# Kernel optimization log

Hardware: AMD Instinct MI355X
Metric: run time of the kernel (lower is better)

The kernel has to match this reference:

```python
import jax, jax.numpy as jnp
import numpy as np

D = 1024           # input_size
D2 = 2 * D         # hidden width of the three inner linears
OUT = 1024         # output_size
S = 8192           # tokens per example


def setup_inputs() -> dict:
    key = jax.random.key(0)
    ks = jax.random.split(key, 11)
    def lin(k, fan_in, fan_out):
        bound = 1.0 / np.sqrt(fan_in)
        kw, kb = jax.random.split(k)
        W = jax.random.uniform(kw, (fan_in, fan_out), jnp.float32, -bound, bound)
        b = jax.random.uniform(kb, (fan_out,), jnp.float32, -bound, bound)
        return W, b
    W_in, b_in = lin(ks[0], D, D2)      # reading_example_input
    W_out, b_out = lin(ks[1], D, D2)    # reading_example_output
    W_cat, b_cat = lin(ks[2], D2, D2)   # concatenated_layer_map
    W_fin, b_fin = lin(ks[3], D2, OUT)  # final_map
    return {
        "input_embedding": jax.random.normal(ks[4], (1, S, D), jnp.float32),
        "output_embedding": jax.random.normal(ks[5], (1, S, D), jnp.float32),
        "random_augmentation": jax.random.normal(ks[6], (1, S, D), jnp.float32),
        "W_in": W_in, "b_in": b_in,
        "W_out": W_out, "b_out": b_out,
        "W_cat": W_cat, "b_cat": b_cat,
        "W_fin": W_fin, "b_fin": b_fin,
    }


def reference(input_embedding, output_embedding, random_augmentation,
              W_in, b_in, W_out, b_out, W_cat, b_cat, W_fin, b_fin):
    def march(x, y):
        # x, y: [1, S, D]
        iq = jax.nn.softmax(x @ W_in + b_in, axis=-1)[0]    # [S, 2D]
        oq = jax.nn.softmax(y @ W_out + b_out, axis=-1)[0]  # [S, 2D]
        cat = jnp.concatenate((x, y), axis=-1)[0]           # [S, 2D]
        icm = jax.nn.softmax(cat @ W_cat + b_cat, axis=-1)  # [S, 2D]
        iqk = iq.T @ icm                                    # [2D, 2D]
        oqk = oq.T @ icm                                    # [2D, 2D]
        meta = jax.nn.relu(iqk @ oqk.T)                     # [2D, 2D]
        scale = jnp.sqrt(jnp.float32(icm.shape[-1]))
        res = (icm @ meta) / scale                          # [S, 2D]
        return jax.nn.relu(res @ W_fin + b_fin)             # [S, OUT]

    transformation = march(input_embedding, output_embedding)
    random_desc = march(input_embedding, random_augmentation)
    return (transformation, random_desc)
```

## Files before the change

### kernel.cpp

```cpp
#include <hip/hip_runtime.h>

#define S_TOK 8192
#define DIM   1024
#define DIM2  2048
#define OUTN  1024

typedef __bf16 bf16x8 __attribute__((ext_vector_type(8)));
typedef float  f32x4  __attribute__((ext_vector_type(4)));
typedef short  s16x8  __attribute__((ext_vector_type(8)));
typedef unsigned short u16x4 __attribute__((ext_vector_type(4)));

__device__ __forceinline__ unsigned short f2bf(float x) {
  unsigned u = __builtin_bit_cast(unsigned, x);
  u = (u + 0x7FFFu + ((u >> 16) & 1u)) >> 16;
  return (unsigned short)u;
}
__device__ __forceinline__ float bf2f(unsigned short u) {
  return __builtin_bit_cast(float, (unsigned)u << 16);
}

__device__ __forceinline__ void gld_lds16(const void* g, void* l) {
  auto* g1 = reinterpret_cast<__attribute__((address_space(1))) unsigned*>(
      (unsigned long long)g);
  auto* l3 = reinterpret_cast<__attribute__((address_space(3))) unsigned*>(
      (unsigned long long)l);
  __builtin_amdgcn_global_load_lds(g1, l3, 16, 0, 0);
}

__device__ __forceinline__ int lds_off(int idx, int k) {
  int b = (idx << 7) + (k << 1);
  b ^= ((idx ^ (idx >> 3)) & 7) << 4;
  return b;
}

struct CvtTab { const float* in[3]; unsigned short* out[3]; };
__global__ __launch_bounds__(256) void cvt_f32_bf16_3(CvtTab t) {
  const float* in = t.in[blockIdx.y];
  unsigned short* out = t.out[blockIdx.y];
  int i = blockIdx.x * 256 + threadIdx.x;
  float4 v = ((const float4*)in)[i];
  u16x4 o;
  o[0] = f2bf(v.x); o[1] = f2bf(v.y); o[2] = f2bf(v.z); o[3] = f2bf(v.w);
  *(u16x4*)(out + (size_t)i * 4) = o;
}

struct WtTab { const float* in[4]; unsigned short* out[4]; int R[4]; int C[4]; };
__global__ __launch_bounds__(256) void transpose_w4(WtTab t) {
  const int z = blockIdx.z;
  const int R = t.R[z], C = t.C[z];
  const int r0 = blockIdx.y << 6, c0 = blockIdx.x << 6;
  if (r0 >= R || c0 >= C) return;
  const float* in = t.in[z];
  unsigned short* out = t.out[z];
  __shared__ unsigned short tl[64 * 64];
  const int tid = threadIdx.x;
#pragma unroll
  for (int i = 0; i < 2; ++i) {
    int ch = tid + (i << 8);
    int r = ch >> 3, c8 = (ch & 7) << 3;
    const float* p = in + (size_t)(r0 + r) * C + c0 + c8;
    float4 a = *(const float4*)p, b = *(const float4*)(p + 4);
    s16x8 w;
    w[0] = (short)f2bf(a.x); w[1] = (short)f2bf(a.y);
    w[2] = (short)f2bf(a.z); w[3] = (short)f2bf(a.w);
    w[4] = (short)f2bf(b.x); w[5] = (short)f2bf(b.y);
    w[6] = (short)f2bf(b.z); w[7] = (short)f2bf(b.w);
    int sw = ((r ^ (r >> 3)) & 7) << 3;
    *(s16x8*)&tl[(r << 6) + (c8 ^ sw)] = w;
  }
  __syncthreads();
#pragma unroll
  for (int i = 0; i < 2; ++i) {
    int ch = tid + (i << 8);
    int c = ch >> 3, r8 = (ch & 7) << 3;
    s16x8 w;
#pragma unroll
    for (int j = 0; j < 8; ++j) {
      int rr = r8 + j;
      w[j] = (short)tl[(rr << 6) + (c ^ (((rr ^ (rr >> 3)) & 7) << 3))];
    }
    *(s16x8*)(out + (size_t)(c0 + c) * R + r0 + r8) = w;
  }
}

struct SmTab { unsigned short* T[6]; };
__global__ __launch_bounds__(512) void softmax_cols(SmTab tab) {
  unsigned short* T = tab.T[blockIdx.y];
  const int tid = threadIdx.x;
  const int colg = tid & 63, seg = tid >> 6;
  const size_t c = ((size_t)blockIdx.x << 6) + colg;
  float m = -1e30f, s = 0.f;
  for (int n = seg; n < DIM2; n += 8) {
    float v = bf2f(T[(size_t)n * S_TOK + c]);
    float mn = fmaxf(m, v);
    s = s * __expf(m - mn) + __expf(v - mn);
    m = mn;
  }
  __shared__ float redm[512], reds[512];
  redm[tid] = m; reds[tid] = s;
  __syncthreads();
  if (seg == 0) {
    float M = m, S = s;
#pragma unroll
    for (int k = 1; k < 8; ++k) {
      float mk = redm[colg + (k << 6)], sk = reds[colg + (k << 6)];
      float mn = fmaxf(M, mk);
      S = S * __expf(M - mn) + sk * __expf(mk - mn);
      M = mn;
    }
    redm[colg] = M; reds[colg] = 1.0f / S;
  }
  __syncthreads();
  m = redm[colg];
  const float inv = reds[colg];
  for (int n = seg; n < DIM2; n += 8) {
    size_t idx = (size_t)n * S_TOK + c;
    T[idx] = f2bf(__expf(bf2f(T[idx]) - m) * inv);
  }
}

struct GPtr {
  const unsigned short* A[6];
  const unsigned short* Arow2[6];
  const unsigned short* B[6];
  const unsigned short* Bk2[6];
  const float* bias[6];
  void* C[6];
  int Ks[6];
  int ldas[6];
};
struct TPar { const unsigned short* src[2]; unsigned short* dst[2]; };

template <int BIAS_ROW, int OUT_BF16, int NZG>
__global__ __launch_bounds__(256, 3) void gemm_nt(GPtr p, TPar tp, int ldb, int ldc,
                                                  float scale, int do_relu) {
  __shared__ __align__(16) char lds[32768];
  const int z = blockIdx.z;
  const int tid  = threadIdx.x;

  if (NZG >= 0 && z >= NZG) {
    const unsigned short* src = tp.src[z - NZG];
    unsigned short* dst = tp.dst[z - NZG];
    unsigned short* tl = (unsigned short*)lds;
    const int nblk = gridDim.x * gridDim.y;
    int bid = blockIdx.y * gridDim.x + blockIdx.x;
    for (int it = bid; it < (DIM2 / 64) * (S_TOK / 64); it += nblk) {
      int tx = it & (S_TOK / 64 - 1), ty = it >> 7;
      int r0 = ty << 6, c0 = tx << 6;
#pragma unroll
      for (int i = 0; i < 2; ++i) {
        int ch = tid + (i << 8);
        int r = ch >> 3, c8 = (ch & 7) << 3;
        s16x8 w = *(const s16x8*)(src + (size_t)(r0 + r) * S_TOK + c0 + c8);
        int sw = ((r ^ (r >> 3)) & 7) << 3;
        *(s16x8*)&tl[(r << 6) + (c8 ^ sw)] = w;
      }
      __syncthreads();
#pragma unroll
      for (int i = 0; i < 2; ++i) {
        int ch = tid + (i << 8);
        int c = ch >> 3, r8 = (ch & 7) << 3;
        s16x8 w;
#pragma unroll
        for (int j = 0; j < 8; ++j) {
          int rr = r8 + j;
          w[j] = (short)tl[(rr << 6) + (c ^ (((rr ^ (rr >> 3)) & 7) << 3))];
        }
        *(s16x8*)(dst + (size_t)(c0 + c) * DIM2 + r0 + r8) = w;
      }
      __syncthreads();
    }
    return;
  }

  char* As = lds;
  char* Bs = lds + 16384;
  const int lane = tid & 63;
  const int wave = tid >> 6;
  const int wm = (wave >> 1) << 6;
  const int wn = (wave & 1) << 6;
  const int m0 = blockIdx.y << 7;
  const int n0 = blockIdx.x << 7;
  const int lda = p.ldas[z];
  const int K = p.Ks[z];

  const unsigned short* Au = p.A[z];
  const unsigned short* B  = p.B[z];
  const float* bias = p.bias[z];
  void* Cv = p.C[z];

  int srow[4], sgk[4];
#pragma unroll
  for (int i = 0; i < 4; ++i) {
    int c = (wave << 8) + (i << 6) + lane;
    int row = c >> 3, kc = c & 7;
    srow[i] = row;
    sgk[i]  = (kc ^ ((row ^ (row >> 3)) & 7)) << 3;
  }

  f32x4 acc[4][4];
#pragma unroll
  for (int i = 0; i < 4; ++i)
#pragma unroll
    for (int j = 0; j < 4; ++j) acc[i][j] = {0.f, 0.f, 0.f, 0.f};

  for (int k0 = 0; k0 < K; k0 += 64) {
#pragma unroll
    for (int i = 0; i < 4; ++i) {
      char* dA = As + (((wave << 2) + i) << 10);
      char* dB = Bs + (((wave << 2) + i) << 10);
      gld_lds16(Au + (size_t)(m0 + srow[i]) * lda + k0 + sgk[i], dA);
      gld_lds16(B  + (size_t)(n0 + srow[i]) * ldb + k0 + sgk[i], dB);
    }
    __syncthreads();
#pragma unroll
    for (int ks = 0; ks < 2; ++ks) {
      bf16x8 af[4], bfr[4];
      int kk = (ks << 5) + ((lane >> 4) << 3);
#pragma unroll
      for (int t = 0; t < 4; ++t) {
        af[t]  = *(const bf16x8*)(As + lds_off(wm + (t << 4) + (lane & 15), kk));
        bfr[t] = *(const bf16x8*)(Bs + lds_off(wn + (t << 4) + (lane & 15), kk));
      }
#pragma unroll
      for (int mt = 0; mt < 4; ++mt)
#pragma unroll
        for (int nt = 0; nt < 4; ++nt)
          acc[mt][nt] = __builtin_amdgcn_mfma_f32_16x16x32_bf16(af[mt], bfr[nt], acc[mt][nt], 0, 0, 0);
    }
    __syncthreads();
  }

  if (OUT_BF16) {
    unsigned short* ct = (unsigned short*)lds;
    __syncthreads();
#pragma unroll
    for (int nt = 0; nt < 4; ++nt) {
      int cl = wn + (nt << 4) + (lane & 15);
      float bcol = (!BIAS_ROW && bias) ? bias[n0 + cl] : 0.0f;
#pragma unroll
      for (int mt = 0; mt < 4; ++mt) {
#pragma unroll
        for (int r = 0; r < 4; ++r) {
          int rl = wm + (mt << 4) + ((lane >> 4) << 2) + r;
          float bv = BIAS_ROW ? (bias ? bias[m0 + rl] : 0.0f) : bcol;
          float v = acc[mt][nt][r] * scale + bv;
          if (do_relu) v = fmaxf(v, 0.0f);
          ct[(rl << 7) + (cl ^ (((rl >> 2) & 3) << 4))] = f2bf(v);
        }
      }
    }
    __syncthreads();
#pragma unroll
    for (int it = 0; it < 8; ++it) {
      int c = (it << 8) + tid;
      int rl = c >> 4, co = (c & 15) << 3;
      s16x8 w = *(const s16x8*)(ct + (rl << 7) + (co ^ (((rl >> 2) & 3) << 4)));
      *(s16x8*)((unsigned short*)Cv + (size_t)(m0 + rl) * ldc + n0 + co) = w;
    }
  } else {
#pragma unroll
    for (int nt = 0; nt < 4; ++nt) {
      int col = n0 + wn + (nt << 4) + (lane & 15);
      float bcol = (!BIAS_ROW && bias) ? bias[col] : 0.0f;
#pragma unroll
      for (int mt = 0; mt < 4; ++mt) {
        f32x4 a = acc[mt][nt];
#pragma unroll
        for (int r = 0; r < 4; ++r) {
          int rowg = m0 + wm + (mt << 4) + ((lane >> 4) << 2) + r;
          float bv = BIAS_ROW ? (bias ? bias[rowg] : 0.0f) : bcol;
          float v = a[r] * scale + bv;
          if (do_relu) v = fmaxf(v, 0.0f);
          ((float*)Cv)[(size_t)rowg * ldc + col] = v;
        }
      }
    }
  }
}

template <int ASPLIT, int BSPLIT, int BIAS_ROW, int OUT_BF16>
__global__ __launch_bounds__(512, 2) void gemm256(GPtr p, int ldb, int ldc,
                                                  float scale, int do_relu,
                                                  int RW, int XW) {
  __shared__ __align__(16) char lds[131072];
  const int z = blockIdx.z;
  const int tid  = threadIdx.x;
  const int lane = tid & 63;
  const int wave = tid >> 6;
  const int wm   = wave >> 2;
  const int wn   = wave & 3;
  const int lda  = p.ldas[z];
  const int K    = p.Ks[z];

  const int gx = gridDim.x;
  const int nper = (gx * gridDim.y) >> 3;
  const int RH = nper / RW;
  int bid = blockIdx.y * gx + blockIdx.x;
  int xcd = bid & 7, j = bid >> 3;
  const int n0 = (RW * (xcd % XW) + (j % RW)) << 8;
  const int m0 = (RH * (xcd / XW) + (j / RW)) << 8;

  const unsigned short* Au = p.A[z];
  int mb = m0;
  if (ASPLIT && m0 >= 2048) { Au = p.Arow2[z]; mb = m0 - 2048; }
  const unsigned short* Bp = p.B[z];
  const float* bias = p.bias[z];
  void* Cv = p.C[z];

  const int NT = K >> 6;

  int srow_[2], skel_[2];
#pragma unroll
  for (int i = 0; i < 2; ++i) {
    int row = (i << 7) + (wave << 4) + (lane >> 2);
    srow_[i] = row;
    skel_[i] = ((lane & 3) ^ ((row >> 1) & 3)) << 3;
  }
  const unsigned short* aB[2];
  const unsigned short* bB[2];
  const unsigned short* b2B[2];
#pragma unroll
  for (int i = 0; i < 2; ++i) {
    aB[i]  = Au + (size_t)(mb + srow_[i]) * lda + skel_[i];
    bB[i]  = Bp + (size_t)(n0 + srow_[i]) * ldb + skel_[i];
    b2B[i] = BSPLIT ? (p.Bk2[z] + (size_t)(n0 + srow_[i]) * ldb + skel_[i] - DIM)
                    : bB[i];
  }

  auto stage_unit = [&](int t, int u) {
    const int k0 = t << 6;
    const int h  = u >> 1;
    char* base = lds + ((t & 1) << 16) + ((u & 1) << 15) + (h << 14) + (wave << 10);
#pragma unroll
    for (int i = 0; i < 2; ++i) {
      const unsigned short* src;
      if (u & 1) src = ((BSPLIT && k0 >= DIM) ? b2B[i] : bB[i]) + k0 + (h << 5);
      else       src = aB[i] + k0 + (h << 5);
      gld_lds16(src, base + (i << 13));
    }
  };

  auto rdA = [&](const char* buf, int h, int mf) -> bf16x8 {
    int row = (wm << 7) + (mf << 4) + (lane & 15);
    int col = (lane >> 4) ^ ((row >> 1) & 3);
    return *(const bf16x8*)(buf + (h << 14) + (row << 6) + (col << 4));
  };
  auto rdB = [&](const char* buf, int h, int nf) -> bf16x8 {
    int row = (wn << 6) + (nf << 4) + (lane & 15);
    int col = (lane >> 4) ^ ((row >> 1) & 3);
    return *(const bf16x8*)(buf + 32768 + (h << 14) + (row << 6) + (col << 4));
  };

  f32x4 acc[8][4];
#pragma unroll
  for (int i = 0; i < 8; ++i)
#pragma unroll
    for (int j2 = 0; j2 < 4; ++j2) acc[i][j2] = {0.f, 0.f, 0.f, 0.f};

  stage_unit(0, 0); stage_unit(0, 1); stage_unit(0, 2); stage_unit(0, 3);

  for (int t = 0; t < NT; ++t) {
    const char* buf = lds + ((t & 1) << 16);
    const bool more = (t + 1 < NT);
    bf16x8 aq[4], bq[4];

    if (more) { stage_unit(t + 1, 0); asm volatile("s_waitcnt vmcnt(6)" ::: "memory"); }
    else      { asm volatile("s_waitcnt vmcnt(4)" ::: "memory"); }
    __builtin_amdgcn_s_barrier();
    __builtin_amdgcn_sched_barrier(0);
#pragma unroll
    for (int nf = 0; nf < 4; ++nf) bq[nf] = rdB(buf, 0, nf);
#pragma unroll
    for (int mf = 0; mf < 4; ++mf) aq[mf] = rdA(buf, 0, mf);
    __builtin_amdgcn_s_setprio(1);
#pragma unroll
    for (int mf = 0; mf < 4; ++mf)
#pragma unroll
      for (int nf = 0; nf < 4; ++nf)
        acc[mf][nf] = __builtin_amdgcn_mfma_f32_16x16x32_bf16(aq[mf], bq[nf], acc[mf][nf], 0, 0, 0);
    __builtin_amdgcn_s_setprio(0);
    __builtin_amdgcn_s_barrier();

#pragma unroll
    for (int mf = 0; mf < 4; ++mf) aq[mf] = rdA(buf, 0, mf + 4);
    if (more) stage_unit(t + 1, 1);
    __builtin_amdgcn_s_setprio(1);
#pragma unroll
    for (int mf = 0; mf < 4; ++mf)
#pragma unroll
      for (int nf = 0; nf < 4; ++nf)
        acc[mf + 4][nf] = __builtin_amdgcn_mfma_f32_16x16x32_bf16(aq[mf], bq[nf], acc[mf + 4][nf], 0, 0, 0);
    __builtin_amdgcn_s_setprio(0);
    __builtin_amdgcn_s_barrier();

    if (more) { stage_unit(t + 1, 2); asm volatile("s_waitcnt vmcnt(6)" ::: "memory"); }
    else      { asm volatile("s_waitcnt vmcnt(0)" ::: "memory"); }
    __builtin_amdgcn_s_barrier();
    __builtin_amdgcn_sched_barrier(0);
#pragma unroll
    for (int nf = 0; nf < 4; ++nf) bq[nf] = rdB(buf, 1, nf);
#pragma unroll
    for (int mf = 0; mf < 4; ++mf) aq[mf] = rdA(buf, 1, mf);
    __builtin_amdgcn_s_setprio(1);
#pragma unroll
    for (int mf = 0; mf < 4; ++mf)
#pragma unroll
      for (int nf = 0; nf < 4; ++nf)
        acc[mf][nf] = __builtin_amdgcn_mfma_f32_16x16x32_bf16(aq[mf], bq[nf], acc[mf][nf], 0, 0, 0);
    __builtin_amdgcn_s_setprio(0);
    __builtin_amdgcn_s_barrier();

#pragma unroll
    for (int mf = 0; mf < 4; ++mf) aq[mf] = rdA(buf, 1, mf + 4);
    if (more) stage_unit(t + 1, 3);
    __builtin_amdgcn_s_setprio(1);
#pragma unroll
    for (int mf = 0; mf < 4; ++mf)
#pragma unroll
      for (int nf = 0; nf < 4; ++nf)
        acc[mf + 4][nf] = __builtin_amdgcn_mfma_f32_16x16x32_bf16(aq[mf], bq[nf], acc[mf + 4][nf], 0, 0, 0);
    __builtin_amdgcn_s_setprio(0);
    __builtin_amdgcn_s_barrier();
  }

  __syncthreads();
  if (OUT_BF16) {
    unsigned short* ct = (unsigned short*)lds;
#pragma unroll
    for (int nf = 0; nf < 4; ++nf) {
      int cl = (wn << 6) + (nf << 4) + (lane & 15);
      float bcol = (!BIAS_ROW && bias) ? bias[n0 + cl] : 0.0f;
#pragma unroll
      for (int mf = 0; mf < 8; ++mf) {
#pragma unroll
        for (int r = 0; r < 4; ++r) {
          int rl = (wm << 7) + (mf << 4) + ((lane >> 4) << 2) + r;
          float bv = BIAS_ROW ? (bias ? bias[m0 + rl] : 0.0f) : bcol;
          float v = acc[mf][nf][r] * scale + bv;
          if (do_relu) v = fmaxf(v, 0.0f);
          ct[(rl << 8) + (cl ^ (((rl >> 2) & 3) << 4))] = f2bf(v);
        }
      }
    }
    __syncthreads();
#pragma unroll
    for (int it = 0; it < 16; ++it) {
      int c = (it << 9) + tid;
      int rl = c >> 5, co = (c & 31) << 3;
      s16x8 w = *(const s16x8*)(ct + (rl << 8) + (co ^ (((rl >> 2) & 3) << 4)));
      *(s16x8*)((unsigned short*)Cv + (size_t)(m0 + rl) * ldc + n0 + co) = w;
    }
  } else {
    float* ctf = (float*)lds;
#pragma unroll
    for (int h = 0; h < 2; ++h) {
      if (h) __syncthreads();
      if (wm == h) {
#pragma unroll
        for (int nf = 0; nf < 4; ++nf) {
          int cl = (wn << 6) + (nf << 4) + (lane & 15);
          float bcol = (!BIAS_ROW && bias) ? bias[n0 + cl] : 0.0f;
#pragma unroll
          for (int mf = 0; mf < 8; ++mf) {
#pragma unroll
            for (int r = 0; r < 4; ++r) {
              int rl2 = (mf << 4) + ((lane >> 4) << 2) + r;
              float bv = BIAS_ROW ? (bias ? bias[m0 + (h << 7) + rl2] : 0.0f) : bcol;
              float v = acc[mf][nf][r] * scale + bv;
              if (do_relu) v = fmaxf(v, 0.0f);
              ctf[(rl2 << 8) + (cl ^ (((rl2 >> 2) & 3) << 3))] = v;
            }
          }
        }
      }
      __syncthreads();
#pragma unroll
      for (int it = 0; it < 16; ++it) {
        int c = (it << 9) + tid;
        int rl2 = c >> 6, co = (c & 63) << 2;
        float4 w = *(const float4*)(ctf + (rl2 << 8) + (co ^ (((rl2 >> 2) & 3) << 3)));
        *(float4*)((float*)Cv + (size_t)(m0 + (h << 7) + rl2) * ldc + n0 + co) = w;
      }
    }
  }
}

extern "C" void kernel_launch(void* const* d_in, const int* in_sizes, int n_in,
                              void* d_out, int out_size, void* d_ws, size_t ws_size,
                              hipStream_t stream) {
  const float* X   = (const float*)d_in[0];
  const float* Y   = (const float*)d_in[1];
  const float* R   = (const float*)d_in[2];
  const float* Wi  = (const float*)d_in[3];
  const float* bi  = (const float*)d_in[4];
  const float* Wo  = (const float*)d_in[5];
  const float* bo  = (const float*)d_in[6];
  const float* Wc  = (const float*)d_in[7];
  const float* bc  = (const float*)d_in[8];
  const float* Wf  = (const float*)d_in[9];
  const float* bf_ = (const float*)d_in[10];
  float* out = (float*)d_out;

  char* ws = (char*)d_ws;
  size_t off = 0;
  auto alloc = [&](size_t b) { char* p = ws + off; off += (b + 255) & ~(size_t)255; return p; };
  unsigned short* Xb   = (unsigned short*)alloc((size_t)S_TOK * DIM  * 2);
  unsigned short* Yb   = (unsigned short*)alloc((size_t)S_TOK * DIM  * 2);
  unsigned short* Rb   = (unsigned short*)alloc((size_t)S_TOK * DIM  * 2);
  unsigned short* WiT  = (unsigned short*)alloc((size_t)DIM2 * DIM  * 2);
  unsigned short* WoT  = (unsigned short*)alloc((size_t)DIM2 * DIM  * 2);
  unsigned short* WcT  = (unsigned short*)alloc((size_t)DIM2 * DIM2 * 2);
  unsigned short* WfT  = (unsigned short*)alloc((size_t)OUTN * DIM2 * 2);
  unsigned short* iqT  = (unsigned short*)alloc((size_t)DIM2 * S_TOK * 2);
  unsigned short* oqT0 = (unsigned short*)alloc((size_t)DIM2 * S_TOK * 2);
  unsigned short* oqT1 = (unsigned short*)alloc((size_t)DIM2 * S_TOK * 2);
  unsigned short* icmT0= (unsigned short*)alloc((size_t)DIM2 * S_TOK * 2);
  unsigned short* icmT1= (unsigned short*)alloc((size_t)DIM2 * S_TOK * 2);
  unsigned short* iqk0 = Xb;
  unsigned short* oqk0 = Xb + (size_t)DIM2*DIM2;
  unsigned short* iqk1 = Yb;
  unsigned short* oqk1 = Yb + (size_t)DIM2*DIM2;
  unsigned short* meta0= iqT;
  unsigned short* meta1= iqT + (size_t)DIM2*DIM2;
  unsigned short* MWT0 = iqT + (size_t)2*DIM2*DIM2;
  unsigned short* MWT1 = iqT + (size_t)2*DIM2*DIM2 + (size_t)OUTN*DIM2;
  unsigned short* icm0 = oqT0;
  unsigned short* icm1 = oqT1;

  {
    CvtTab t{};
    t.in[0] = X; t.in[1] = Y; t.in[2] = R;
    t.out[0] = Xb; t.out[1] = Yb; t.out[2] = Rb;
    cvt_f32_bf16_3<<<dim3((S_TOK * DIM / 4) / 256, 3), 256, 0, stream>>>(t);
  }
  {
    WtTab t{};
    t.in[0] = Wi; t.out[0] = WiT; t.R[0] = DIM;  t.C[0] = DIM2;
    t.in[1] = Wo; t.out[1] = WoT; t.R[1] = DIM;  t.C[1] = DIM2;
    t.in[2] = Wc; t.out[2] = WcT; t.R[2] = DIM2; t.C[2] = DIM2;
    t.in[3] = Wf; t.out[3] = WfT; t.R[3] = DIM2; t.C[3] = OUTN;
    transpose_w4<<<dim3(32, 32, 4), 256, 0, stream>>>(t);
  }

  const float rscale = 0.022097086912079608f;

  {
    GPtr g{};
    g.A[0] = WcT; g.B[0] = Xb; g.Bk2[0] = Yb; g.bias[0] = bc; g.C[0] = icmT0;
    g.Ks[0] = DIM2; g.ldas[0] = DIM2;
    g.A[1] = WcT; g.B[1] = Xb; g.Bk2[1] = Rb; g.bias[1] = bc; g.C[1] = icmT1;
    g.Ks[1] = DIM2; g.ldas[1] = DIM2;
    g.A[2] = WiT; g.B[2] = Xb; g.Bk2[2] = Xb; g.bias[2] = bi; g.C[2] = iqT;
    g.Ks[2] = DIM; g.ldas[2] = DIM;
    g.A[3] = WoT; g.B[3] = Yb; g.Bk2[3] = Yb; g.bias[3] = bo; g.C[3] = oqT0;
    g.Ks[3] = DIM; g.ldas[3] = DIM;
    g.A[4] = WoT; g.B[4] = Rb; g.Bk2[4] = Rb; g.bias[4] = bo; g.C[4] = oqT1;
    g.Ks[4] = DIM; g.ldas[4] = DIM;
    gemm256<0,1,1,1><<<dim3(S_TOK/256, DIM2/256, 5), 512, 0, stream>>>(
        g, DIM, S_TOK, 1.f, 0, 4, 8);
  }
  {
    SmTab st{};
    st.T[0] = iqT; st.T[1] = oqT0; st.T[2] = oqT1; st.T[3] = icmT0; st.T[4] = icmT1;
    softmax_cols<<<dim3(S_TOK / 64, 5), dim3(512), 0, stream>>>(st);
  }
  {
    GPtr g{};
    g.A[0] = iqT; g.A[1] = iqT;
    g.Arow2[0] = oqT0; g.Arow2[1] = oqT1;
    g.B[0] = icmT0; g.B[1] = icmT1;
    g.C[0] = iqk0; g.C[1] = iqk1;
    g.Ks[0] = S_TOK; g.Ks[1] = S_TOK;
    g.ldas[0] = S_TOK; g.ldas[1] = S_TOK;
    gemm256<1,0,0,1><<<dim3(DIM2/256, 4096/256, 2), 512, 0, stream>>>(
        g, S_TOK, DIM2, 1.f, 0, 4, 2);
  }
  {
    GPtr g{};
    g.A[0] = iqk0; g.B[0] = oqk0; g.C[0] = meta0; g.Ks[0] = DIM2; g.ldas[0] = DIM2;
    g.A[1] = iqk1; g.B[1] = oqk1; g.C[1] = meta1; g.Ks[1] = DIM2; g.ldas[1] = DIM2;
    TPar tp{};
    tp.src[0] = icmT0; tp.dst[0] = icm0;
    tp.src[1] = icmT1; tp.dst[1] = icm1;
    gemm_nt<0,1,2><<<dim3(DIM2/128, DIM2/128, 4), 256, 0, stream>>>(
        g, tp, DIM2, DIM2, 1.f, 1);
  }
  {
    GPtr g{};
    g.A[0] = WfT; g.B[0] = meta0; g.C[0] = MWT0; g.Ks[0] = DIM2; g.ldas[0] = DIM2;
    g.A[1] = WfT; g.B[1] = meta1; g.C[1] = MWT1; g.Ks[1] = DIM2; g.ldas[1] = DIM2;
    TPar tp{};
    gemm_nt<0,1,2><<<dim3(DIM2/128, OUTN/128, 2), 256, 0, stream>>>(
        g, tp, DIM2, DIM2, rscale, 0);
  }
  {
    GPtr g{};
    g.A[0] = icm0; g.B[0] = MWT0; g.bias[0] = bf_; g.C[0] = out;
    g.Ks[0] = DIM2; g.ldas[0] = DIM2;
    g.A[1] = icm1; g.B[1] = MWT1; g.bias[1] = bf_;
    g.C[1] = out + (size_t)S_TOK * OUTN;
    g.Ks[1] = DIM2; g.ldas[1] = DIM2;
    gemm256<0,0,0,0><<<dim3(OUTN/256, S_TOK/256, 2), 512, 0, stream>>>(
        g, DIM2, OUTN, 1.f, 1, 4, 1);
  }
  (void)in_sizes; (void)n_in; (void)out_size; (void)ws_size;
}
```

Before: 893.0 us.

## Merge prep kernels, cache softmax column values, add two-phase GEMM pipeline variant

Fuses the activation bf16 conversion and the weight transpose into one launch to save a kernel launch. The column softmax now keeps its loaded values in registers (32 x 8 bf16 per thread), so the normalisation pass does not re-read global memory. A PHASES template parameter adds a two-phase main-loop schedule to the first projection GEMM, with fewer barriers and larger register fragments; the other GEMMs keep the four-phase schedule. The risks are higher register pressure in softmax and in the two-phase GEMM, and a mostly idle grid in the merged prep kernel.

```diff
diff --git a/kernel.cpp b/kernel.cpp
--- a/kernel.cpp
+++ b/kernel.cpp
@@ -33,27 +33,31 @@
   return b;
 }
 
-struct CvtTab { const float* in[3]; unsigned short* out[3]; };
-__global__ __launch_bounds__(256) void cvt_f32_bf16_3(CvtTab t) {
-  const float* in = t.in[blockIdx.y];
-  unsigned short* out = t.out[blockIdx.y];
-  int i = blockIdx.x * 256 + threadIdx.x;
-  float4 v = ((const float4*)in)[i];
-  u16x4 o;
-  o[0] = f2bf(v.x); o[1] = f2bf(v.y); o[2] = f2bf(v.z); o[3] = f2bf(v.w);
-  *(u16x4*)(out + (size_t)i * 4) = o;
-}
-
-struct WtTab { const float* in[4]; unsigned short* out[4]; int R[4]; int C[4]; };
-__global__ __launch_bounds__(256) void transpose_w4(WtTab t) {
-  const int z = blockIdx.z;
-  const int R = t.R[z], C = t.C[z];
-  const int r0 = blockIdx.y << 6, c0 = blockIdx.x << 6;
-  if (r0 >= R || c0 >= C) return;
-  const float* in = t.in[z];
-  unsigned short* out = t.out[z];
+struct PrepTab {
+  const float* in[3]; unsigned short* out[3];
+  const float* win[4]; unsigned short* wout[4]; int R[4]; int C[4];
+};
+__global__ __launch_bounds__(256) void prep_all(PrepTab t) {
   __shared__ unsigned short tl[64 * 64];
   const int tid = threadIdx.x;
+  if (blockIdx.z < 3) {
+    const float* in = t.in[blockIdx.z];
+    unsigned short* out = t.out[blockIdx.z];
+    int i = blockIdx.x * 256 + tid;
+    float4 v = ((const float4*)in)[i];
+    u16x4 o;
+    o[0] = f2bf(v.x); o[1] = f2bf(v.y); o[2] = f2bf(v.z); o[3] = f2bf(v.w);
+    *(u16x4*)(out + (size_t)i * 4) = o;
+    return;
+  }
+  int x = blockIdx.x;
+  if (x >= 4096) return;
+  int wz = x >> 10, rem = x & 1023, bx = rem & 31, by = rem >> 5;
+  const int R = t.R[wz], C = t.C[wz];
+  const int r0 = by << 6, c0 = bx << 6;
+  if (r0 >= R || c0 >= C) return;
+  const float* in = t.win[wz];
+  unsigned short* out = t.wout[wz];
 #pragma unroll
   for (int i = 0; i < 2; ++i) {
     int ch = tid + (i << 8);
@@ -89,12 +93,22 @@
   const int tid = threadIdx.x;
   const int colg = tid & 63, seg = tid >> 6;
   const size_t c = ((size_t)blockIdx.x << 6) + colg;
+  s16x8 cache[32];
   float m = -1e30f, s = 0.f;
-  for (int n = seg; n < DIM2; n += 8) {
-    float v = bf2f(T[(size_t)n * S_TOK + c]);
-    float mn = fmaxf(m, v);
-    s = s * __expf(m - mn) + __expf(v - mn);
-    m = mn;
+#pragma unroll
+  for (int k = 0; k < 32; ++k) {
+    s16x8 v;
+#pragma unroll
+    for (int j = 0; j < 8; ++j) {
+      int n = seg + (((k << 3) + j) << 3);
+      unsigned short u = T[(size_t)n * S_TOK + c];
+      v[j] = (short)u;
+      float f = bf2f(u);
+      float mn = fmaxf(m, f);
+      s = s * __expf(m - mn) + __expf(f - mn);
+      m = mn;
+    }
+    cache[k] = v;
   }
   __shared__ float redm[512], reds[512];
   redm[tid] = m; reds[tid] = s;
@@ -113,9 +127,14 @@
   __syncthreads();
   m = redm[colg];
   const float inv = reds[colg];
-  for (int n = seg; n < DIM2; n += 8) {
-    size_t idx = (size_t)n * S_TOK + c;
-    T[idx] = f2bf(__expf(bf2f(T[idx]) - m) * inv);
+#pragma unroll
+  for (int k = 0; k < 32; ++k) {
+#pragma unroll
+    for (int j = 0; j < 8; ++j) {
+      int n = seg + (((k << 3) + j) << 3);
+      T[(size_t)n * S_TOK + c] =
+          f2bf(__expf(bf2f((unsigned short)cache[k][j]) - m) * inv);
+    }
   }
 }
 
@@ -279,7 +298,7 @@
   }
 }
 
-template <int ASPLIT, int BSPLIT, int BIAS_ROW, int OUT_BF16>
+template <int ASPLIT, int BSPLIT, int BIAS_ROW, int OUT_BF16, int PHASES>
 __global__ __launch_bounds__(512, 2) void gemm256(GPtr p, int ldb, int ldc,
                                                   float scale, int do_relu,
                                                   int RW, int XW) {
@@ -363,65 +382,106 @@
   for (int t = 0; t < NT; ++t) {
     const char* buf = lds + ((t & 1) << 16);
     const bool more = (t + 1 < NT);
-    bf16x8 aq[4], bq[4];
-
-    if (more) { stage_unit(t + 1, 0); asm volatile("s_waitcnt vmcnt(6)" ::: "memory"); }
-    else      { asm volatile("s_waitcnt vmcnt(4)" ::: "memory"); }
-    __builtin_amdgcn_s_barrier();
-    __builtin_amdgcn_sched_barrier(0);
-#pragma unroll
-    for (int nf = 0; nf < 4; ++nf) bq[nf] = rdB(buf, 0, nf);
-#pragma unroll
-    for (int mf = 0; mf < 4; ++mf) aq[mf] = rdA(buf, 0, mf);
-    __builtin_amdgcn_s_setprio(1);
-#pragma unroll
-    for (int mf = 0; mf < 4; ++mf)
-#pragma unroll
-      for (int nf = 0; nf < 4; ++nf)
-        acc[mf][nf] = __builtin_amdgcn_mfma_f32_16x16x32_bf16(aq[mf], bq[nf], acc[mf][nf], 0, 0, 0);
-    __builtin_amdgcn_s_setprio(0);
-    __builtin_amdgcn_s_barrier();
-
-#pragma unroll
-    for (int mf = 0; mf < 4; ++mf) aq[mf] = rdA(buf, 0, mf + 4);
-    if (more) stage_unit(t + 1, 1);
-    __builtin_amdgcn_s_setprio(1);
-#pragma unroll
-    for (int mf = 0; mf < 4; ++mf)
-#pragma unroll
-      for (int nf = 0; nf < 4; ++nf)
-        acc[mf + 4][nf] = __builtin_amdgcn_mfma_f32_16x16x32_bf16(aq[mf], bq[nf], acc[mf + 4][nf], 0, 0, 0);
-    __builtin_amdgcn_s_setprio(0);
-    __builtin_amdgcn_s_barrier();
-
-    if (more) { stage_unit(t + 1, 2); asm volatile("s_waitcnt vmcnt(6)" ::: "memory"); }
-    else      { asm volatile("s_waitcnt vmcnt(0)" ::: "memory"); }
-    __builtin_amdgcn_s_barrier();
-    __builtin_amdgcn_sched_barrier(0);
-#pragma unroll
-    for (int nf = 0; nf < 4; ++nf) bq[nf] = rdB(buf, 1, nf);
-#pragma unroll
-    for (int mf = 0; mf < 4; ++mf) aq[mf] = rdA(buf, 1, mf);
-    __builtin_amdgcn_s_setprio(1);
-#pragma unroll
-    for (int mf = 0; mf < 4; ++mf)
-#pragma unroll
-      for (int nf = 0; nf < 4; ++nf)
-        acc[mf][nf] = __builtin_amdgcn_mfma_f32_16x16x32_bf16(aq[mf], bq[nf], acc[mf][nf], 0, 0, 0);
-    __builtin_amdgcn_s_setprio(0);
-    __builtin_amdgcn_s_barrier();
-
-#pragma unroll
-    for (int mf = 0; mf < 4; ++mf) aq[mf] = rdA(buf, 1, mf + 4);
-    if (more) stage_unit(t + 1, 3);
-    __builtin_amdgcn_s_setprio(1);
-#pragma unroll
-    for (int mf = 0; mf < 4; ++mf)
-#pragma unroll
-      for (int nf = 0; nf < 4; ++nf)
-        acc[mf + 4][nf] = __builtin_amdgcn_mfma_f32_16x16x32_bf16(aq[mf], bq[nf], acc[mf + 4][nf], 0, 0, 0);
-    __builtin_amdgcn_s_setprio(0);
-    __builtin_amdgcn_s_barrier();
+
+    if (PHASES == 2) {
+      bf16x8 aq[8], bq[4];
+      if (more) {
+        stage_unit(t + 1, 0); stage_unit(t + 1, 1);
+        asm volatile("s_waitcnt vmcnt(8)" ::: "memory");
+      } else {
+        asm volatile("s_waitcnt vmcnt(4)" ::: "memory");
+      }
+      __builtin_amdgcn_s_barrier();
+      __builtin_amdgcn_sched_barrier(0);
+#pragma unroll
+      for (int nf = 0; nf < 4; ++nf) bq[nf] = rdB(buf, 0, nf);
+#pragma unroll
+      for (int mf = 0; mf < 8; ++mf) aq[mf] = rdA(buf, 0, mf);
+      __builtin_amdgcn_s_setprio(1);
+#pragma unroll
+      for (int mf = 0; mf < 8; ++mf)
+#pragma unroll
+        for (int nf = 0; nf < 4; ++nf)
+          acc[mf][nf] = __builtin_amdgcn_mfma_f32_16x16x32_bf16(aq[mf], bq[nf], acc[mf][nf], 0, 0, 0);
+      __builtin_amdgcn_s_setprio(0);
+      __builtin_amdgcn_s_barrier();
+      if (more) {
+        stage_unit(t + 1, 2); stage_unit(t + 1, 3);
+        asm volatile("s_waitcnt vmcnt(8)" ::: "memory");
+      } else {
+        asm volatile("s_waitcnt vmcnt(0)" ::: "memory");
+      }
+      __builtin_amdgcn_s_barrier();
+      __builtin_amdgcn_sched_barrier(0);
+#pragma unroll
+      for (int nf = 0; nf < 4; ++nf) bq[nf] = rdB(buf, 1, nf);
+#pragma unroll
+      for (int mf = 0; mf < 8; ++mf) aq[mf] = rdA(buf, 1, mf);
+      __builtin_amdgcn_s_setprio(1);
+#pragma unroll
+      for (int mf = 0; mf < 8; ++mf)
+#pragma unroll
+        for (int nf = 0; nf < 4; ++nf)
+          acc[mf][nf] = __builtin_amdgcn_mfma_f32_16x16x32_bf16(aq[mf], bq[nf], acc[mf][nf], 0, 0, 0);
+      __builtin_amdgcn_s_setprio(0);
+      __builtin_amdgcn_s_barrier();
+    } else {
+      bf16x8 aq[4], bq[4];
+      if (more) { stage_unit(t + 1, 0); asm volatile("s_waitcnt vmcnt(6)" ::: "memory"); }
+      else      { asm volatile("s_waitcnt vmcnt(4)" ::: "memory"); }
+      __builtin_amdgcn_s_barrier();
+      __builtin_amdgcn_sched_barrier(0);
+#pragma unroll
+      for (int nf = 0; nf < 4; ++nf) bq[nf] = rdB(buf, 0, nf);
+#pragma unroll
+      for (int mf = 0; mf < 4; ++mf) aq[mf] = rdA(buf, 0, mf);
+      __builtin_amdgcn_s_setprio(1);
+#pragma unroll
+      for (int mf = 0; mf < 4; ++mf)
+#pragma unroll
+        for (int nf = 0; nf < 4; ++nf)
+          acc[mf][nf] = __builtin_amdgcn_mfma_f32_16x16x32_bf16(aq[mf], bq[nf], acc[mf][nf], 0, 0, 0);
+      __builtin_amdgcn_s_setprio(0);
+      __builtin_amdgcn_s_barrier();
+#pragma unroll
+      for (int mf = 0; mf < 4; ++mf) aq[mf] = rdA(buf, 0, mf + 4);
+      if (more) stage_unit(t + 1, 1);
+      __builtin_amdgcn_s_setprio(1);
+#pragma unroll
+      for (int mf = 0; mf < 4; ++mf)
+#pragma unroll
+        for (int nf = 0; nf < 4; ++nf)
+          acc[mf + 4][nf] = __builtin_amdgcn_mfma_f32_16x16x32_bf16(aq[mf], bq[nf], acc[mf + 4][nf], 0, 0, 0);
+      __builtin_amdgcn_s_setprio(0);
+      __builtin_amdgcn_s_barrier();
+      if (more) { stage_unit(t + 1, 2); asm volatile("s_waitcnt vmcnt(6)" ::: "memory"); }
+      else      { asm volatile("s_waitcnt vmcnt(0)" ::: "memory"); }
+      __builtin_amdgcn_s_barrier();
+      __builtin_amdgcn_sched_barrier(0);
+#pragma unroll
+      for (int nf = 0; nf < 4; ++nf) bq[nf] = rdB(buf, 1, nf);
+#pragma unroll
+      for (int mf = 0; mf < 4; ++mf) aq[mf] = rdA(buf, 1, mf);
+      __builtin_amdgcn_s_setprio(1);
+#pragma unroll
+      for (int mf = 0; mf < 4; ++mf)
+#pragma unroll
+        for (int nf = 0; nf < 4; ++nf)
+          acc[mf][nf] = __builtin_amdgcn_mfma_f32_16x16x32_bf16(aq[mf], bq[nf], acc[mf][nf], 0, 0, 0);
+      __builtin_amdgcn_s_setprio(0);
+      __builtin_amdgcn_s_barrier();
+#pragma unroll
+      for (int mf = 0; mf < 4; ++mf) aq[mf] = rdA(buf, 1, mf + 4);
+      if (more) stage_unit(t + 1, 3);
+      __builtin_amdgcn_s_setprio(1);
+#pragma unroll
+      for (int mf = 0; mf < 4; ++mf)
+#pragma unroll
+        for (int nf = 0; nf < 4; ++nf)
+          acc[mf + 4][nf] = __builtin_amdgcn_mfma_f32_16x16x32_bf16(aq[mf], bq[nf], acc[mf + 4][nf], 0, 0, 0);
+      __builtin_amdgcn_s_setprio(0);
+      __builtin_amdgcn_s_barrier();
+    }
   }
 
   __syncthreads();
@@ -529,18 +589,14 @@
   unsigned short* icm1 = oqT1;
 
   {
-    CvtTab t{};
+    PrepTab t{};
     t.in[0] = X; t.in[1] = Y; t.in[2] = R;
     t.out[0] = Xb; t.out[1] = Yb; t.out[2] = Rb;
-    cvt_f32_bf16_3<<<dim3((S_TOK * DIM / 4) / 256, 3), 256, 0, stream>>>(t);
-  }
-  {
-    WtTab t{};
-    t.in[0] = Wi; t.out[0] = WiT; t.R[0] = DIM;  t.C[0] = DIM2;
-    t.in[1] = Wo; t.out[1] = WoT; t.R[1] = DIM;  t.C[1] = DIM2;
-    t.in[2] = Wc; t.out[2] = WcT; t.R[2] = DIM2; t.C[2] = DIM2;
-    t.in[3] = Wf; t.out[3] = WfT; t.R[3] = DIM2; t.C[3] = OUTN;
-    transpose_w4<<<dim3(32, 32, 4), 256, 0, stream>>>(t);
+    t.win[0] = Wi; t.wout[0] = WiT; t.R[0] = DIM;  t.C[0] = DIM2;
+    t.win[1] = Wo; t.wout[1] = WoT; t.R[1] = DIM;  t.C[1] = DIM2;
+    t.win[2] = Wc; t.wout[2] = WcT; t.R[2] = DIM2; t.C[2] = DIM2;
+    t.win[3] = Wf; t.wout[3] = WfT; t.R[3] = DIM2; t.C[3] = OUTN;
+    prep_all<<<dim3((S_TOK * DIM / 4) / 256, 1, 4), 256, 0, stream>>>(t);
   }
 
   const float rscale = 0.022097086912079608f;
@@ -557,7 +613,7 @@
     g.Ks[3] = DIM; g.ldas[3] = DIM;
     g.A[4] = WoT; g.B[4] = Rb; g.Bk2[4] = Rb; g.bias[4] = bo; g.C[4] = oqT1;
     g.Ks[4] = DIM; g.ldas[4] = DIM;
-    gemm256<0,1,1,1><<<dim3(S_TOK/256, DIM2/256, 5), 512, 0, stream>>>(
+    gemm256<0,1,1,1,2><<<dim3(S_TOK/256, DIM2/256, 5), 512, 0, stream>>>(
         g, DIM, S_TOK, 1.f, 0, 4, 8);
   }
   {
@@ -573,7 +629,7 @@
     g.C[0] = iqk0; g.C[1] = iqk1;
     g.Ks[0] = S_TOK; g.Ks[1] = S_TOK;
     g.ldas[0] = S_TOK; g.ldas[1] = S_TOK;
-    gemm256<1,0,0,1><<<dim3(DIM2/256, 4096/256, 2), 512, 0, stream>>>(
+    gemm256<1,0,0,1,4><<<dim3(DIM2/256, 4096/256, 2), 512, 0, stream>>>(
         g, S_TOK, DIM2, 1.f, 0, 4, 2);
   }
   {
@@ -601,7 +657,7 @@
     g.A[1] = icm1; g.B[1] = MWT1; g.bias[1] = bf_;
     g.C[1] = out + (size_t)S_TOK * OUTN;
     g.Ks[1] = DIM2; g.ldas[1] = DIM2;
-    gemm256<0,0,0,0><<<dim3(OUTN/256, S_TOK/256, 2), 512, 0, stream>>>(
+    gemm256<0,0,0,0,4><<<dim3(OUTN/256, S_TOK/256, 2), 512, 0, stream>>>(
         g, DIM2, OUTN, 1.f, 1, 4, 1);
   }
   (void)in_sizes; (void)n_in; (void)out_size; (void)ws_size;
```

New measurement: 1.506 ms. 68.7% more time.
